# Kernel optimization log

Hardware: AMD Instinct MI355X
Metric: run time of the kernel (lower is better)

## Reference

```python
import jax, jax.numpy as jnp
import numpy as np

N_EMBD = 768
N_HEAD = 12
HEAD_SIZE = 64  # n_embd // n_head
LN_EPS = 1e-5


def layer_norm(x, g, b):
    mu = jnp.mean(x, axis=-1, keepdims=True)
    var = jnp.var(x, axis=-1, keepdims=True)
    return (x - mu) * jax.lax.rsqrt(var + LN_EPS) * g + b


def setup_inputs() -> dict:
    key = jax.random.key(0)
    ks = jax.random.split(key, 12)
    B, T, C, H, D = 4, 2048, N_EMBD, N_HEAD, HEAD_SIZE
    s = 0.02
    return {
        "x": jax.random.normal(ks[0], (B, T, C), jnp.float32),
        "wq": jax.random.normal(ks[1], (H, C, D), jnp.float32) * s,
        "wk": jax.random.normal(ks[2], (H, C, D), jnp.float32) * s,
        "wv": jax.random.normal(ks[3], (H, C, D), jnp.float32) * s,
        "w_proj": jax.random.normal(ks[4], (C, C), jnp.float32) * s,
        "b_proj": jnp.zeros((C,), jnp.float32),
        "w1": jax.random.normal(ks[5], (C, 4 * C), jnp.float32) * s,
        "b1": jnp.zeros((4 * C,), jnp.float32),
        "w2": jax.random.normal(ks[6], (4 * C, C), jnp.float32) * s,
        "b2": jnp.zeros((C,), jnp.float32),
        "ln1_g": jnp.ones((C,), jnp.float32),
        "ln1_b": jnp.zeros((C,), jnp.float32),
        "ln2_g": jnp.ones((C,), jnp.float32),
        "ln2_b": jnp.zeros((C,), jnp.float32),
    }


def reference(x, wq, wk, wv, w_proj, b_proj, w1, b1, w2, b2,
              ln1_g, ln1_b, ln2_g, ln2_b):
    B, T, C = x.shape
    # --- self-attention sublayer (dropout in eval mode -> identity) ---
    h = layer_norm(x, ln1_g, ln1_b)
    q = jnp.einsum('btc,hcd->bhtd', h, wq)
    k = jnp.einsum('btc,hcd->bhtd', h, wk)
    v = jnp.einsum('btc,hcd->bhtd', h, wv)
    scores = jnp.einsum('bhtd,bhsd->bhts', q, k) * (HEAD_SIZE ** -0.5)
    causal = jnp.tril(jnp.ones((T, T), bool))
    scores = jnp.where(causal, scores, -jnp.inf)
    attn = jax.nn.softmax(scores, axis=-1)  # [B,H,T,T]
    out = jnp.einsum('bhts,bhsd->bhtd', attn, v)
    out = out.transpose(0, 2, 1, 3).reshape(B, T, C)  # concat heads
    x = x + out @ w_proj + b_proj
    # --- FFN sublayer ---
    h2 = layer_norm(x, ln2_g, ln2_b)
    x = x + jax.nn.relu(h2 @ w1 + b1) @ w2 + b2
    return x
```

## Files before the change

### kernel.cpp

```cpp
#include <hip/hip_runtime.h>
#include <hip/hip_bf16.h>

typedef __attribute__((ext_vector_type(8))) short bf16x8;
typedef __attribute__((ext_vector_type(4))) short bf16x4;
typedef __attribute__((ext_vector_type(4))) float f32x4;

#define AS1 __attribute__((address_space(1)))
#define AS3 __attribute__((address_space(3)))

__global__ __launch_bounds__(256)
void ln_kernel(const float* __restrict__ x, const float* __restrict__ g,
               const float* __restrict__ b, __hip_bfloat16* __restrict__ out)
{
    const int wave = threadIdx.x >> 6, lane = threadIdx.x & 63;
    const int row = blockIdx.x * 4 + wave;
    const float* xr = x + (size_t)row * 768;
    float4 v[3];
#pragma unroll
    for (int j = 0; j < 3; j++)
        v[j] = *(const float4*)(xr + lane * 4 + 256 * j);
    float s = 0.f, ss = 0.f;
#pragma unroll
    for (int j = 0; j < 3; j++) {
        s  += (v[j].x + v[j].y) + (v[j].z + v[j].w);
        ss += (v[j].x * v[j].x + v[j].y * v[j].y) +
              (v[j].z * v[j].z + v[j].w * v[j].w);
    }
#pragma unroll
    for (int off = 1; off < 64; off <<= 1) {
        s  += __shfl_xor(s, off, 64);
        ss += __shfl_xor(ss, off, 64);
    }
    const float mu = s * (1.0f / 768.0f);
    const float rstd = rsqrtf(ss * (1.0f / 768.0f) - mu * mu + 1e-5f);
    __hip_bfloat16* orow = out + (size_t)row * 768;
#pragma unroll
    for (int j = 0; j < 3; j++) {
        const int c = lane * 4 + 256 * j;
        const float4 gv = *(const float4*)(g + c);
        const float4 bv = *(const float4*)(b + c);
        bf16x4 pk;
        __hip_bfloat16* pp = (__hip_bfloat16*)&pk;
        pp[0] = __float2bfloat16((v[j].x - mu) * rstd * gv.x + bv.x);
        pp[1] = __float2bfloat16((v[j].y - mu) * rstd * gv.y + bv.y);
        pp[2] = __float2bfloat16((v[j].z - mu) * rstd * gv.z + bv.z);
        pp[3] = __float2bfloat16((v[j].w - mu) * rstd * gv.w + bv.w);
        *(bf16x4*)(orow + c) = pk;
    }
}

__global__ __launch_bounds__(256)
void weight_prep(const float* __restrict__ wq, const float* __restrict__ wk,
                 const float* __restrict__ wv, const float* __restrict__ w_proj,
                 const float* __restrict__ w1, const float* __restrict__ w2,
                 __hip_bfloat16* __restrict__ o_qkv,
                 __hip_bfloat16* __restrict__ o_proj,
                 __hip_bfloat16* __restrict__ o_w1,
                 __hip_bfloat16* __restrict__ o_w2)
{
    __shared__ float tile[32][33];
    const int tx = threadIdx.x, ty = threadIdx.y;
    int id = blockIdx.x;
    const float* in; __hip_bfloat16* out;
    int R, C, r0, c0;
    if (id < 1728) {
        const int ct = id % 24, dt = (id / 24) % 2, z = id / 48;
        const int mat = z / 12, h = z % 12;
        const float* w = (mat == 0) ? wq : ((mat == 1) ? wk : wv);
        const int c0v = ct * 32, d0 = dt * 32;
#pragma unroll
        for (int i = 0; i < 4; i++)
            tile[ty + i * 8][tx] =
                w[(size_t)h * 768 * 64 + (size_t)(c0v + ty + i * 8) * 64 + d0 + tx];
        __syncthreads();
#pragma unroll
        for (int i = 0; i < 4; i++)
            o_qkv[(size_t)(mat * 768 + h * 64 + d0 + ty + i * 8) * 768 + c0v + tx] =
                __float2bfloat16(tile[tx][ty + i * 8]);
        return;
    } else if (id < 2304) {
        id -= 1728; in = w_proj; out = o_proj; R = 768; C = 768;
        c0 = (id % 24) * 32; r0 = (id / 24) * 32;
    } else if (id < 4608) {
        id -= 2304; in = w1; out = o_w1; R = 768; C = 3072;
        c0 = (id % 96) * 32; r0 = (id / 96) * 32;
    } else {
        id -= 4608; in = w2; out = o_w2; R = 3072; C = 768;
        c0 = (id % 24) * 32; r0 = (id / 24) * 32;
    }
#pragma unroll
    for (int i = 0; i < 4; i++)
        tile[ty + i * 8][tx] = in[(size_t)(r0 + ty + i * 8) * C + c0 + tx];
    __syncthreads();
#pragma unroll
    for (int i = 0; i < 4; i++)
        out[(size_t)(c0 + ty + i * 8) * R + r0 + tx] =
            __float2bfloat16(tile[tx][ty + i * 8]);
}

template<int MODE>
__global__ __launch_bounds__(256)
void gemm_kernel(const __hip_bfloat16* __restrict__ A,
                 const __hip_bfloat16* __restrict__ Bt,
                 const float* __restrict__ bias,
                 const float* __restrict__ res,
                 void* __restrict__ outp,
                 __hip_bfloat16* __restrict__ outK,
                 __hip_bfloat16* __restrict__ outV,
                 int M, int N, int K)
{
    __shared__ alignas(16) char As[128 * 128];
    __shared__ alignas(16) char Bs[128 * 128];
    const int tid = threadIdx.x;
    const int wave = tid >> 6, lane = tid & 63;

    const int nwgx = gridDim.x;
    const int hw = blockIdx.x + nwgx * blockIdx.y;
    const int nwg = nwgx * gridDim.y;
    const int q8 = nwg >> 3;
    const int work = (hw & 7) * q8 + (hw >> 3);
    const int m0 = (work / nwgx) * 128, n0 = (work % nwgx) * 128;

    const int wm = (wave >> 1) * 64, wn = (wave & 1) * 64;
    f32x4 acc[4][4] = {};

    int soff[4];
#pragma unroll
    for (int r = 0; r < 4; r++) {
        const int n = tid + 256 * r;
        const int row = n >> 3;
        soff[r] = row * (K * 2) + ((((n & 7) << 4)) ^ ((row & 7) << 4));
    }

    const int fr = lane & 15, fg = lane >> 4;

    for (int k0 = 0; k0 < K; k0 += 64) {
        __syncthreads();
        const char* ga = (const char*)A  + (size_t)m0 * K * 2 + k0 * 2;
        const char* gb = (const char*)Bt + (size_t)n0 * K * 2 + k0 * 2;
#pragma unroll
        for (int r = 0; r < 4; r++) {
            __builtin_amdgcn_global_load_lds((const AS1 void*)(ga + soff[r]),
                (AS3 void*)(As + r * 4096 + tid * 16), 16, 0, 0);
            __builtin_amdgcn_global_load_lds((const AS1 void*)(gb + soff[r]),
                (AS3 void*)(Bs + r * 4096 + tid * 16), 16, 0, 0);
        }
        __syncthreads();
        bf16x8 af[4][2], bfr[4][2];
#pragma unroll
        for (int i = 0; i < 4; i++)
#pragma unroll
            for (int ks = 0; ks < 2; ks++)
                af[i][ks] = *(const bf16x8*)(As + (wm + i * 16 + fr) * 128 +
                            ((fg * 16 + ks * 64) ^ ((fr & 7) << 4)));
#pragma unroll
        for (int j = 0; j < 4; j++)
#pragma unroll
            for (int ks = 0; ks < 2; ks++)
                bfr[j][ks] = *(const bf16x8*)(Bs + (wn + j * 16 + fr) * 128 +
                             ((fg * 16 + ks * 64) ^ ((fr & 7) << 4)));
        __builtin_amdgcn_s_setprio(1);
#pragma unroll
        for (int ks = 0; ks < 2; ks++)
#pragma unroll
            for (int i = 0; i < 4; i++)
#pragma unroll
                for (int j = 0; j < 4; j++)
                    acc[i][j] = __builtin_amdgcn_mfma_f32_16x16x32_bf16(
                        af[i][ks], bfr[j][ks], acc[i][j], 0, 0, 0);
        __builtin_amdgcn_s_setprio(0);
    }

#pragma unroll
    for (int j = 0; j < 4; j++) {
        const int n = n0 + wn + j * 16 + fr;
        if (MODE == 1 && n >= 1536) {
            const int hh = (n - 1536) >> 6, dd = (n - 1536) & 63;
#pragma unroll
            for (int i = 0; i < 4; i++) {
                const int m = m0 + wm + i * 16 + fg * 4;
                const int bidx = m >> 11, tt = m & 2047;
                bf16x4 pk;
                __hip_bfloat16* pp = (__hip_bfloat16*)&pk;
#pragma unroll
                for (int r = 0; r < 4; r++)
                    pp[r] = __float2bfloat16(acc[i][j][r]);
                *(bf16x4*)&outV[(((size_t)bidx * 12 + hh) * 64 + dd) * 2048 + tt] = pk;
            }
            continue;
        }
        const float bv = (MODE == 2 || MODE == 3) ? bias[n] : 0.0f;
#pragma unroll
        for (int i = 0; i < 4; i++) {
#pragma unroll
            for (int r = 0; r < 4; r++) {
                const int m = m0 + wm + i * 16 + fg * 4 + r;
                float v = acc[i][j][r] + bv;
                if (MODE == 3) v = fmaxf(v, 0.0f);
                if (MODE == 2) {
                    ((float*)outp)[(size_t)m * N + n] = res[(size_t)m * N + n] + v;
                } else if (MODE == 1) {
                    __hip_bfloat16* dst; int nc;
                    if (n < 768) { dst = (__hip_bfloat16*)outp; nc = n;
                                   v *= 0.18033688011112042f;  }
                    else         { dst = outK; nc = n - 768; }
                    const int hh = nc >> 6, dd = nc & 63;
                    const int bidx = m >> 11, tt = m & 2047;
                    dst[(((size_t)bidx * 12 + hh) * 2048 + tt) * 64 + dd] =
                        __float2bfloat16(v);
                } else {
                    ((__hip_bfloat16*)outp)[(size_t)m * N + n] = __float2bfloat16(v);
                }
            }
        }
    }
}

__global__ __launch_bounds__(256)
void attn_kernel(const __hip_bfloat16* __restrict__ Q,
                 const __hip_bfloat16* __restrict__ Kg,
                 const __hip_bfloat16* __restrict__ Vg,
                 __hip_bfloat16* __restrict__ out)
{
    __shared__ alignas(16) char lds[32768];
    const int tid = threadIdx.x, wave = tid >> 6, lane = tid & 63;
    const int fr = lane & 15, fg = lane >> 4;

    const int hw = blockIdx.x + 16 * blockIdx.y;
    const int xcd = hw & 7, chunk = hw >> 3;
    const int bh = xcd * 6 + (chunk >> 4);
    const int bx = chunk & 15;

    const int b = bh / 12, h = bh % 12;
    const __hip_bfloat16* qb = Q  + (size_t)bh * 2048 * 64;
    const __hip_bfloat16* kb = Kg + (size_t)bh * 2048 * 64;
    const __hip_bfloat16* vb = Vg + (size_t)bh * 2048 * 64;

    int ksoff[2], vsoff[2];
#pragma unroll
    for (int r = 0; r < 2; r++) {
        const int n = wave * 64 + lane + 256 * r;
        const int row = n >> 3;
        const int swz = (((n & 7) << 4)) ^ ((row & 7) << 4);
        ksoff[r] = row * 128  + swz;
        vsoff[r] = row * 4096 + swz;
    }

    auto STAGE = [&](int cur, int kv0) {
        const char* kx = (const char*)kb + (size_t)kv0 * 128;
        const char* vx = (const char*)vb + (size_t)kv0 * 2;
#pragma unroll
        for (int r = 0; r < 2; r++) {
            __builtin_amdgcn_global_load_lds((const AS1 void*)(kx + ksoff[r]),
                (AS3 void*)(lds + cur * 16384 + r * 4096 + wave * 1024), 16, 0, 0);
            __builtin_amdgcn_global_load_lds((const AS1 void*)(vx + vsoff[r]),
                (AS3 void*)(lds + cur * 16384 + 8192 + r * 4096 + wave * 1024), 16, 0, 0);
        }
    };

    const bf16x4 ones = {(short)0x3F80, (short)0x3F80,
                         (short)0x3F80, (short)0x3F80};

#pragma unroll
    for (int pass = 0; pass < 2; ++pass) {
        const int g = pass ? (31 - bx) : bx;
        const int q0w = g * 64 + wave * 16;
        const int qv = q0w + fr;

        bf16x8 qf0 = *(const bf16x8*)(qb + (size_t)qv * 64 + fg * 8);
        bf16x8 qf1 = *(const bf16x8*)(qb + (size_t)qv * 64 + 32 + fg * 8);

        f32x4 o[4] = {};
        f32x4 o_l = {};
        float mrun = -1e30f;
        const int NT = g + 1;

        STAGE(0, 0);
        __syncthreads();
        int cur = 0;

        for (int t = 0; t < NT; ++t) {
            if (t + 1 < NT) STAGE(cur ^ 1, (t + 1) << 6);
            const int kv0 = t << 6;
            const char* Kb = lds + cur * 16384;
            const char* Vb = Kb + 8192;
            bf16x8 kf[4][2];
#pragma unroll
            for (int c = 0; c < 4; c++)
#pragma unroll
                for (int hh = 0; hh < 2; hh++)
                    kf[c][hh] = *(const bf16x8*)(Kb + (16 * c + fr) * 128 +
                                ((hh * 64 + fg * 16) ^ ((fr & 7) << 4)));
            f32x4 s[4];
            __builtin_amdgcn_s_setprio(1);
#pragma unroll
            for (int c = 0; c < 4; c++) {
                f32x4 z = {};
                s[c] = __builtin_amdgcn_mfma_f32_16x16x32_bf16(
                    kf[c][0], qf0, z, 0, 0, 0);
                s[c] = __builtin_amdgcn_mfma_f32_16x16x32_bf16(
                    kf[c][1], qf1, s[c], 0, 0, 0);
            }
            __builtin_amdgcn_s_setprio(0);
            if (t == NT - 1) {
#pragma unroll
                for (int c = 0; c < 4; c++)
#pragma unroll
                    for (int r = 0; r < 4; r++)
                        if (kv0 + 16 * c + 4 * fg + r > qv) s[c][r] = -1e30f;
            }
            float t0 = fmaxf(fmaxf(s[0][0], s[0][1]), fmaxf(s[0][2], s[0][3]));
            float t1 = fmaxf(fmaxf(s[1][0], s[1][1]), fmaxf(s[1][2], s[1][3]));
            float t2 = fmaxf(fmaxf(s[2][0], s[2][1]), fmaxf(s[2][2], s[2][3]));
            float t3 = fmaxf(fmaxf(s[3][0], s[3][1]), fmaxf(s[3][2], s[3][3]));
            const float tm = fmaxf(fmaxf(t0, t1), fmaxf(t2, t3));
            if (!__all(tm <= mrun + 8.f)) {
                float tf = fmaxf(tm, __shfl_xor(tm, 16, 64));
                tf = fmaxf(tf, __shfl_xor(tf, 32, 64));
                const float mnew = fmaxf(mrun, tf);
                const float al = exp2f(mrun - mnew);
#pragma unroll
                for (int i = 0; i < 4; i++)
#pragma unroll
                    for (int e = 0; e < 4; e++) o[i][e] *= al;
#pragma unroll
                for (int e = 0; e < 4; e++) o_l[e] *= al;
                mrun = mnew;
            }
            bf16x4 pf[4];
#pragma unroll
            for (int c = 0; c < 4; c++) {
                const float p0 = exp2f(s[c][0] - mrun), p1 = exp2f(s[c][1] - mrun);
                const float p2 = exp2f(s[c][2] - mrun), p3 = exp2f(s[c][3] - mrun);
                __hip_bfloat16* pp = (__hip_bfloat16*)&pf[c];
                pp[0] = __float2bfloat16(p0); pp[1] = __float2bfloat16(p1);
                pp[2] = __float2bfloat16(p2); pp[3] = __float2bfloat16(p3);
            }
            bf16x4 vf[4][4];
#pragma unroll
            for (int i = 0; i < 4; i++)
#pragma unroll
                for (int c = 0; c < 4; c++)
                    vf[i][c] = *(const bf16x4*)(Vb + (16 * i + fr) * 128 +
                                ((32 * c + 8 * fg) ^ ((fr & 7) << 4)));
            __builtin_amdgcn_s_setprio(1);
#pragma unroll
            for (int c = 0; c < 4; c++)
                o_l = __builtin_amdgcn_mfma_f32_16x16x16bf16_1k(
                    ones, pf[c], o_l, 0, 0, 0);
#pragma unroll
            for (int i = 0; i < 4; i++)
#pragma unroll
                for (int c = 0; c < 4; c++)
                    o[i] = __builtin_amdgcn_mfma_f32_16x16x16bf16_1k(
                        vf[i][c], pf[c], o[i], 0, 0, 0);
            __builtin_amdgcn_s_setprio(0);
            __syncthreads();
            cur ^= 1;
        }

        const float inv = 1.0f / o_l[0];
        __hip_bfloat16* ob = out + ((size_t)(b * 2048 + qv)) * 768 + h * 64;
#pragma unroll
        for (int i = 0; i < 4; i++) {
            bf16x4 pk;
            __hip_bfloat16* pp = (__hip_bfloat16*)&pk;
#pragma unroll
            for (int r = 0; r < 4; r++)
                pp[r] = __float2bfloat16(o[i][r] * inv);
            *(bf16x4*)(ob + 16 * i + 4 * fg) = pk;
        }
    }
}

extern "C" void kernel_launch(void* const* d_in, const int* in_sizes, int n_in,
                              void* d_out, int out_size, void* d_ws, size_t ws_size,
                              hipStream_t stream)
{
    const float* x      = (const float*)d_in[0];
    const float* wq     = (const float*)d_in[1];
    const float* wk     = (const float*)d_in[2];
    const float* wv     = (const float*)d_in[3];
    const float* w_proj = (const float*)d_in[4];
    const float* b_proj = (const float*)d_in[5];
    const float* w1     = (const float*)d_in[6];
    const float* b1     = (const float*)d_in[7];
    const float* w2     = (const float*)d_in[8];
    const float* b2     = (const float*)d_in[9];
    const float* ln1_g  = (const float*)d_in[10];
    const float* ln1_b  = (const float*)d_in[11];
    const float* ln2_g  = (const float*)d_in[12];
    const float* ln2_b  = (const float*)d_in[13];
    float* out = (float*)d_out;

    char* w = (char*)d_ws;
    size_t off = 0;
    auto alloc = [&](size_t bytes) {
        void* p = w + off;
        off += (bytes + 255) & ~(size_t)255;
        return p;
    };
    __hip_bfloat16* h_ln    = (__hip_bfloat16*)alloc(8192ull * 768 * 2);
    __hip_bfloat16* wt_qkv  = (__hip_bfloat16*)alloc(2304ull * 768 * 2);
    __hip_bfloat16* wt_proj = (__hip_bfloat16*)alloc(768ull * 768 * 2);
    __hip_bfloat16* wt1     = (__hip_bfloat16*)alloc(3072ull * 768 * 2);
    __hip_bfloat16* wt2     = (__hip_bfloat16*)alloc(768ull * 3072 * 2);
    __hip_bfloat16* qbuf    = (__hip_bfloat16*)alloc(8192ull * 768 * 2);
    __hip_bfloat16* kbuf    = (__hip_bfloat16*)alloc(8192ull * 768 * 2);
    __hip_bfloat16* vbuf    = (__hip_bfloat16*)alloc(8192ull * 768 * 2);
    __hip_bfloat16* attn_o  = (__hip_bfloat16*)alloc(8192ull * 768 * 2);
    float*          x1      = (float*)alloc(8192ull * 768 * 4);
    __hip_bfloat16* h2      = (__hip_bfloat16*)alloc(8192ull * 768 * 2);
    __hip_bfloat16* a1      = qbuf;

    weight_prep<<<6912, dim3(32, 8), 0, stream>>>(
        wq, wk, wv, w_proj, w1, w2, wt_qkv, wt_proj, wt1, wt2);

    ln_kernel<<<2048, 256, 0, stream>>>(x, ln1_g, ln1_b, h_ln);
    gemm_kernel<1><<<dim3(18, 64), 256, 0, stream>>>(
        h_ln, wt_qkv, nullptr, nullptr, qbuf, kbuf, vbuf, 8192, 2304, 768);
    attn_kernel<<<dim3(16, 48), 256, 0, stream>>>(qbuf, kbuf, vbuf, attn_o);
    gemm_kernel<2><<<dim3(6, 64), 256, 0, stream>>>(
        attn_o, wt_proj, b_proj, x, x1, nullptr, nullptr, 8192, 768, 768);

    ln_kernel<<<2048, 256, 0, stream>>>(x1, ln2_g, ln2_b, h2);
    gemm_kernel<3><<<dim3(24, 64), 256, 0, stream>>>(
        h2, wt1, b1, nullptr, a1, nullptr, nullptr, 8192, 3072, 768);
    gemm_kernel<2><<<dim3(6, 64), 256, 0, stream>>>(
        a1, wt2, b2, x1, out, nullptr, nullptr, 8192, 768, 3072);
}
```

Baseline: 241.3 us.

## Use 128x96 GEMM tiles for narrow GEMMs and store residual x1 in bf16

Adds a BN template parameter so the QKV, projection and FFN2 GEMMs use 128x96 output tiles. This raises the workgroup count for the N=768 GEMMs from 384 to 512, giving better coverage of the compute units. The intermediate residual x1 is now stored in bf16 instead of fp32, which cuts memory traffic in the projection epilogue, the second layernorm and the FFN2 residual read. The cost is lower precision on the residual path and less data reuse per tile.

```diff
diff --git a/kernel.cpp b/kernel.cpp
--- a/kernel.cpp
+++ b/kernel.cpp
@@ -8,24 +8,36 @@
 #define AS1 __attribute__((address_space(1)))
 #define AS3 __attribute__((address_space(3)))
 
+template<bool BF16IN>
 __global__ __launch_bounds__(256)
-void ln_kernel(const float* __restrict__ x, const float* __restrict__ g,
+void ln_kernel(const void* __restrict__ xin, const float* __restrict__ g,
                const float* __restrict__ b, __hip_bfloat16* __restrict__ out)
 {
     const int wave = threadIdx.x >> 6, lane = threadIdx.x & 63;
     const int row = blockIdx.x * 4 + wave;
-    const float* xr = x + (size_t)row * 768;
-    float4 v[3];
+    float v[3][4];
+    if (BF16IN) {
+        const __hip_bfloat16* xr = (const __hip_bfloat16*)xin + (size_t)row * 768;
+#pragma unroll
+        for (int j = 0; j < 3; j++) {
+            bf16x4 t = *(const bf16x4*)(xr + lane * 4 + 256 * j);
+#pragma unroll
+            for (int k = 0; k < 4; k++)
+                v[j][k] = __bfloat162float(((const __hip_bfloat16*)&t)[k]);
+        }
+    } else {
+        const float* xr = (const float*)xin + (size_t)row * 768;
+#pragma unroll
+        for (int j = 0; j < 3; j++) {
+            float4 t = *(const float4*)(xr + lane * 4 + 256 * j);
+            v[j][0] = t.x; v[j][1] = t.y; v[j][2] = t.z; v[j][3] = t.w;
+        }
+    }
+    float s = 0.f, ss = 0.f;
 #pragma unroll
     for (int j = 0; j < 3; j++)
-        v[j] = *(const float4*)(xr + lane * 4 + 256 * j);
-    float s = 0.f, ss = 0.f;
-#pragma unroll
-    for (int j = 0; j < 3; j++) {
-        s  += (v[j].x + v[j].y) + (v[j].z + v[j].w);
-        ss += (v[j].x * v[j].x + v[j].y * v[j].y) +
-              (v[j].z * v[j].z + v[j].w * v[j].w);
-    }
+#pragma unroll
+        for (int k = 0; k < 4; k++) { s += v[j][k]; ss += v[j][k] * v[j][k]; }
 #pragma unroll
     for (int off = 1; off < 64; off <<= 1) {
         s  += __shfl_xor(s, off, 64);
@@ -41,10 +53,10 @@
         const float4 bv = *(const float4*)(b + c);
         bf16x4 pk;
         __hip_bfloat16* pp = (__hip_bfloat16*)&pk;
-        pp[0] = __float2bfloat16((v[j].x - mu) * rstd * gv.x + bv.x);
-        pp[1] = __float2bfloat16((v[j].y - mu) * rstd * gv.y + bv.y);
-        pp[2] = __float2bfloat16((v[j].z - mu) * rstd * gv.z + bv.z);
-        pp[3] = __float2bfloat16((v[j].w - mu) * rstd * gv.w + bv.w);
+        pp[0] = __float2bfloat16((v[j][0] - mu) * rstd * gv.x + bv.x);
+        pp[1] = __float2bfloat16((v[j][1] - mu) * rstd * gv.y + bv.y);
+        pp[2] = __float2bfloat16((v[j][2] - mu) * rstd * gv.z + bv.z);
+        pp[3] = __float2bfloat16((v[j][3] - mu) * rstd * gv.w + bv.w);
         *(bf16x4*)(orow + c) = pk;
     }
 }
@@ -98,19 +110,20 @@
             __float2bfloat16(tile[tx][ty + i * 8]);
 }
 
-template<int MODE>
+template<int MODE, int BN>
 __global__ __launch_bounds__(256)
 void gemm_kernel(const __hip_bfloat16* __restrict__ A,
                  const __hip_bfloat16* __restrict__ Bt,
                  const float* __restrict__ bias,
-                 const float* __restrict__ res,
+                 const void* __restrict__ res,
                  void* __restrict__ outp,
                  __hip_bfloat16* __restrict__ outK,
                  __hip_bfloat16* __restrict__ outV,
                  int M, int N, int K)
 {
+    constexpr int NREP = BN / 32;
     __shared__ alignas(16) char As[128 * 128];
-    __shared__ alignas(16) char Bs[128 * 128];
+    __shared__ alignas(16) char Bs[BN * 128];
     const int tid = threadIdx.x;
     const int wave = tid >> 6, lane = tid & 63;
 
@@ -119,10 +132,10 @@
     const int nwg = nwgx * gridDim.y;
     const int q8 = nwg >> 3;
     const int work = (hw & 7) * q8 + (hw >> 3);
-    const int m0 = (work / nwgx) * 128, n0 = (work % nwgx) * 128;
-
-    const int wm = (wave >> 1) * 64, wn = (wave & 1) * 64;
-    f32x4 acc[4][4] = {};
+    const int m0 = (work / nwgx) * 128, n0 = (work % nwgx) * BN;
+
+    const int wm = (wave >> 1) * 64, wn = (wave & 1) * (BN / 2);
+    f32x4 acc[4][NREP] = {};
 
     int soff[4];
 #pragma unroll
@@ -139,14 +152,15 @@
         const char* ga = (const char*)A  + (size_t)m0 * K * 2 + k0 * 2;
         const char* gb = (const char*)Bt + (size_t)n0 * K * 2 + k0 * 2;
 #pragma unroll
-        for (int r = 0; r < 4; r++) {
+        for (int r = 0; r < 4; r++)
             __builtin_amdgcn_global_load_lds((const AS1 void*)(ga + soff[r]),
                 (AS3 void*)(As + r * 4096 + tid * 16), 16, 0, 0);
+#pragma unroll
+        for (int r = 0; r < NREP; r++)
             __builtin_amdgcn_global_load_lds((const AS1 void*)(gb + soff[r]),
                 (AS3 void*)(Bs + r * 4096 + tid * 16), 16, 0, 0);
-        }
         __syncthreads();
-        bf16x8 af[4][2], bfr[4][2];
+        bf16x8 af[4][2], bfr[NREP][2];
 #pragma unroll
         for (int i = 0; i < 4; i++)
 #pragma unroll
@@ -154,7 +168,7 @@
                 af[i][ks] = *(const bf16x8*)(As + (wm + i * 16 + fr) * 128 +
                             ((fg * 16 + ks * 64) ^ ((fr & 7) << 4)));
 #pragma unroll
-        for (int j = 0; j < 4; j++)
+        for (int j = 0; j < NREP; j++)
 #pragma unroll
             for (int ks = 0; ks < 2; ks++)
                 bfr[j][ks] = *(const bf16x8*)(Bs + (wn + j * 16 + fr) * 128 +
@@ -165,14 +179,14 @@
 #pragma unroll
             for (int i = 0; i < 4; i++)
 #pragma unroll
-                for (int j = 0; j < 4; j++)
+                for (int j = 0; j < NREP; j++)
                     acc[i][j] = __builtin_amdgcn_mfma_f32_16x16x32_bf16(
                         af[i][ks], bfr[j][ks], acc[i][j], 0, 0, 0);
         __builtin_amdgcn_s_setprio(0);
     }
 
 #pragma unroll
-    for (int j = 0; j < 4; j++) {
+    for (int j = 0; j < NREP; j++) {
         const int n = n0 + wn + j * 16 + fr;
         if (MODE == 1 && n >= 1536) {
             const int hh = (n - 1536) >> 6, dd = (n - 1536) & 63;
@@ -189,7 +203,7 @@
             }
             continue;
         }
-        const float bv = (MODE == 2 || MODE == 3) ? bias[n] : 0.0f;
+        const float bv = (MODE >= 2) ? bias[n] : 0.0f;
 #pragma unroll
         for (int i = 0; i < 4; i++) {
 #pragma unroll
@@ -198,7 +212,11 @@
                 float v = acc[i][j][r] + bv;
                 if (MODE == 3) v = fmaxf(v, 0.0f);
                 if (MODE == 2) {
-                    ((float*)outp)[(size_t)m * N + n] = res[(size_t)m * N + n] + v;
+                    ((__hip_bfloat16*)outp)[(size_t)m * N + n] = __float2bfloat16(
+                        ((const float*)res)[(size_t)m * N + n] + v);
+                } else if (MODE == 4) {
+                    ((float*)outp)[(size_t)m * N + n] =
+                        __bfloat162float(((const __hip_bfloat16*)res)[(size_t)m * N + n]) + v;
                 } else if (MODE == 1) {
                     __hip_bfloat16* dst; int nc;
                     if (n < 768) { dst = (__hip_bfloat16*)outp; nc = n;
@@ -409,23 +427,23 @@
     __hip_bfloat16* kbuf    = (__hip_bfloat16*)alloc(8192ull * 768 * 2);
     __hip_bfloat16* vbuf    = (__hip_bfloat16*)alloc(8192ull * 768 * 2);
     __hip_bfloat16* attn_o  = (__hip_bfloat16*)alloc(8192ull * 768 * 2);
-    float*          x1      = (float*)alloc(8192ull * 768 * 4);
+    __hip_bfloat16* x1      = (__hip_bfloat16*)alloc(8192ull * 768 * 2);
     __hip_bfloat16* h2      = (__hip_bfloat16*)alloc(8192ull * 768 * 2);
     __hip_bfloat16* a1      = qbuf;
 
     weight_prep<<<6912, dim3(32, 8), 0, stream>>>(
         wq, wk, wv, w_proj, w1, w2, wt_qkv, wt_proj, wt1, wt2);
 
-    ln_kernel<<<2048, 256, 0, stream>>>(x, ln1_g, ln1_b, h_ln);
-    gemm_kernel<1><<<dim3(18, 64), 256, 0, stream>>>(
+    ln_kernel<false><<<2048, 256, 0, stream>>>(x, ln1_g, ln1_b, h_ln);
+    gemm_kernel<1, 96><<<dim3(24, 64), 256, 0, stream>>>(
         h_ln, wt_qkv, nullptr, nullptr, qbuf, kbuf, vbuf, 8192, 2304, 768);
     attn_kernel<<<dim3(16, 48), 256, 0, stream>>>(qbuf, kbuf, vbuf, attn_o);
-    gemm_kernel<2><<<dim3(6, 64), 256, 0, stream>>>(
+    gemm_kernel<2, 96><<<dim3(8, 64), 256, 0, stream>>>(
         attn_o, wt_proj, b_proj, x, x1, nullptr, nullptr, 8192, 768, 768);
 
-    ln_kernel<<<2048, 256, 0, stream>>>(x1, ln2_g, ln2_b, h2);
-    gemm_kernel<3><<<dim3(24, 64), 256, 0, stream>>>(
+    ln_kernel<true><<<2048, 256, 0, stream>>>(x1, ln2_g, ln2_b, h2);
+    gemm_kernel<3, 128><<<dim3(24, 64), 256, 0, stream>>>(
         h2, wt1, b1, nullptr, a1, nullptr, nullptr, 8192, 3072, 768);
-    gemm_kernel<2><<<dim3(6, 64), 256, 0, stream>>>(
+    gemm_kernel<4, 96><<<dim3(8, 64), 256, 0, stream>>>(
         a1, wt2, b2, x1, out, nullptr, nullptr, 8192, 768, 3072);
 }
```

Result: faster. 235.0 us (-2.6%).
